# Kernel tuning notes

Measured on AMD Instinct MI355X. Metric: run time of the kernel, lower is better.

## Reference

```python
import jax, jax.numpy as jnp
import numpy as np

K_HOPS = 2  # num_layers in NewSGConv


def setup_inputs() -> dict:
    key = jax.random.key(0)
    ks = jax.random.split(key, 5)
    B, N, F, H, C = 2048, 64, 256, 512, 2
    n_tril = N * (N + 1) // 2  # 2080
    X = jax.random.normal(ks[0], (B, N, F), dtype=jnp.float32)
    edge_weight_tril = jax.random.normal(ks[1], (n_tril,), dtype=jnp.float32) * 0.1
    conv_W = jax.random.normal(ks[2], (F, H), dtype=jnp.float32) * (1.0 / np.sqrt(F))
    conv_b = jnp.zeros((H,), dtype=jnp.float32)
    fc_W = jax.random.normal(ks[3], (C, H), dtype=jnp.float32) * (1.0 / np.sqrt(H))
    fc_b = jnp.zeros((C,), dtype=jnp.float32)
    return {"X": X, "edge_weight_tril": edge_weight_tril, "conv_W": conv_W,
            "conv_b": conv_b, "fc_W": fc_W, "fc_b": fc_b}


def reference(X, edge_weight_tril, conv_W, conv_b, fc_W, fc_b):
    # X: [B, N, F] ; graph is fully connected over N nodes, shared across batch.
    N = X.shape[1]
    xs, ys = jnp.tril_indices(N)
    # Rebuild symmetric dense weight matrix from lower-triangular learnable params
    W = jnp.zeros((N, N), dtype=X.dtype).at[xs, ys].set(edge_weight_tril)
    W = W + W.T - jnp.diag(jnp.diag(W))
    # NewSGConv norm: add self-loops (fill=1), deg from abs(edge_weight)
    A = W + jnp.eye(N, dtype=X.dtype)                 # W_sym + I (extra self-loop edge)
    deg = jnp.abs(W).sum(axis=1) + 1.0                # abs of self-loop weight = 1
    dinv = jnp.where(deg > 0, deg ** -0.5, 0.0)
    An = dinv[:, None] * A * dinv[None, :]            # D^-1/2 (W_sym + I) D^-1/2
    # K-hop SGConv propagation (dense graph -> batched matmul is the exact math)
    x = X
    for _ in range(K_HOPS):
        x = jnp.einsum('nm,bmf->bnf', An, x)
    # SGConv linear, then ReLU (as in model forward)
    h = jax.nn.relu(jnp.einsum('bnf,fh->bnh', x, conv_W) + conv_b)  # [B,N,H]
    # global_add_pool over nodes per graph
    pooled = h.sum(axis=1)                            # [B, H]
    # dropout is identity in eval; final fc + log_softmax
    logits = pooled @ fc_W.T + fc_b                   # [B, C]
    return jax.nn.log_softmax(logits, axis=-1)
```

## Files before the change

### kernel.cpp

```cpp
#include <hip/hip_runtime.h>

typedef float f32x4 __attribute__((ext_vector_type(4)));
typedef short bf16x8 __attribute__((ext_vector_type(8)));

__device__ __forceinline__ short f2bf(float x) {
    unsigned u = __float_as_uint(x);
    unsigned r = (u + 0x7FFFu + ((u >> 16) & 1u)) >> 16;
    return (short)r;
}

__global__ void prep_an2(const float* __restrict__ tril, short* __restrict__ an2f) {
    __shared__ float Wm[64][64];
    __shared__ float An[64][64];
    __shared__ float An2[64][64];
    __shared__ float dinv[64];
    const int t = threadIdx.x;
    for (int e = t; e < 4096; e += 256) {
        int i = e >> 6, j = e & 63;
        int hi = i > j ? i : j, lo = i > j ? j : i;
        Wm[i][j] = tril[hi * (hi + 1) / 2 + lo];
    }
    __syncthreads();
    if (t < 64) {
        float s = 0.f;
        for (int j = 0; j < 64; ++j) s += fabsf(Wm[t][j]);
        s += 1.0f;
        dinv[t] = (s > 0.f) ? 1.0f / sqrtf(s) : 0.f;
    }
    __syncthreads();
    for (int e = t; e < 4096; e += 256) {
        int i = e >> 6, j = e & 63;
        float a = Wm[i][j] + (i == j ? 1.0f : 0.0f);
        An[i][j] = dinv[i] * a * dinv[j];
    }
    __syncthreads();
    for (int e = t; e < 4096; e += 256) {
        int i = e >> 6, j = e & 63;
        float acc = 0.f;
        for (int m = 0; m < 64; ++m) acc += An[i][m] * An[m][j];
        An2[i][j] = acc;
    }
    __syncthreads();
    for (int o = t; o < 4096; o += 256) {
        int e = o & 7, lane = (o >> 3) & 63, kt = (o >> 9) & 1, mt = o >> 10;
        int m = mt * 16 + (lane & 15);
        int k = kt * 32 + 8 * (lane >> 4) + e;
        an2f[o] = f2bf(An2[m][k]);
    }
}

__global__ void prep_wf(const float* __restrict__ convW, short* __restrict__ wf) {
    int o = blockIdx.x * 256 + threadIdx.x;
    int e = o & 7, lane = (o >> 3) & 63, nt = (o >> 9) & 31, kt = o >> 14;
    int k = kt * 32 + 8 * (lane >> 4) + e;
    int j = nt * 16 + (lane & 15);
    wf[o] = f2bf(convW[k * 512 + j]);
}

__global__ __launch_bounds__(256, 2) void rgnn_main(
    const float* __restrict__ X, const short* __restrict__ an2f,
    const short* __restrict__ wf, const float* __restrict__ convb,
    const float* __restrict__ fcW, const float* __restrict__ fcb,
    float* __restrict__ out)
{
    __shared__ short xbuf[16384];
    __shared__ short an2lds[4096];
    __shared__ float pooled[512];
    const int b = blockIdx.x;
    const int t = threadIdx.x;
    const int lane = t & 63;
    const int wid = t >> 6;
    const float* Xb = X + (size_t)b * (64 * 256);

    {
        bf16x8 a0 = *(const bf16x8*)&an2f[t * 16];
        bf16x8 a1 = *(const bf16x8*)&an2f[t * 16 + 8];
        *(bf16x8*)&an2lds[t * 16] = a0;
        *(bf16x8*)&an2lds[t * 16 + 8] = a1;
    }
    {
        const int c = t;
        #pragma unroll 2
        for (int m0 = 0; m0 < 64; m0 += 8) {
            bf16x8 v;
            #pragma unroll
            for (int i = 0; i < 8; ++i) v[i] = f2bf(Xb[(m0 + i) * 256 + c]);
            int byte = c * 128 + m0 * 2;
            byte ^= (c & 7) << 4;
            *(bf16x8*)((char*)xbuf + byte) = v;
        }
    }
    __syncthreads();

    f32x4 acc_a[4][4];
    {
        const int c0 = wid * 64;
        #pragma unroll
        for (int mt = 0; mt < 4; ++mt)
            #pragma unroll
            for (int nt = 0; nt < 4; ++nt) acc_a[mt][nt] = (f32x4)0.f;
        #pragma unroll
        for (int kt = 0; kt < 2; ++kt) {
            #pragma unroll
            for (int nt = 0; nt < 4; ++nt) {
                int row = c0 + nt * 16 + (lane & 15);
                int byte = row * 128 + (kt * 32 + 8 * (lane >> 4)) * 2;
                byte ^= (row & 7) << 4;
                bf16x8 bfr = *(const bf16x8*)((const char*)xbuf + byte);
                #pragma unroll
                for (int mt = 0; mt < 4; ++mt) {
                    bf16x8 afr = *(const bf16x8*)&an2lds[((mt * 2 + kt) * 64 + lane) * 8];
                    acc_a[mt][nt] = __builtin_amdgcn_mfma_f32_16x16x32_bf16(afr, bfr, acc_a[mt][nt], 0, 0, 0);
                }
            }
        }
    }
    __syncthreads();

    {
        const int c0 = wid * 64;
        #pragma unroll
        for (int mt = 0; mt < 4; ++mt)
            #pragma unroll
            for (int nt = 0; nt < 4; ++nt)
                #pragma unroll
                for (int r = 0; r < 4; ++r) {
                    int row = mt * 16 + (lane >> 4) * 4 + r;
                    int col = c0 + nt * 16 + (lane & 15);
                    int byte = row * 512 + col * 2;
                    byte ^= (row & 7) << 4;
                    *(short*)((char*)xbuf + byte) = f2bf(acc_a[mt][nt][r]);
                }
    }
    __syncthreads();

    #pragma unroll 1
    for (int half = 0; half < 2; ++half) {
        const int j0 = wid * 128 + half * 64;
        f32x4 acc[4][4];
        #pragma unroll
        for (int mt = 0; mt < 4; ++mt)
            #pragma unroll
            for (int nt = 0; nt < 4; ++nt) acc[mt][nt] = (f32x4)0.f;
        #pragma unroll
        for (int kt = 0; kt < 8; ++kt) {
            bf16x8 bfr[4];
            #pragma unroll
            for (int nt = 0; nt < 4; ++nt) {
                int ntg = (j0 >> 4) + nt;
                bfr[nt] = *(const bf16x8*)&wf[((kt * 32 + ntg) * 64 + lane) * 8];
            }
            #pragma unroll
            for (int mt = 0; mt < 4; ++mt) {
                int row = mt * 16 + (lane & 15);
                int byte = row * 512 + (kt * 32 + 8 * (lane >> 4)) * 2;
                byte ^= (row & 7) << 4;
                bf16x8 afrb = *(const bf16x8*)((const char*)xbuf + byte);
                #pragma unroll
                for (int nt = 0; nt < 4; ++nt)
                    acc[mt][nt] = __builtin_amdgcn_mfma_f32_16x16x32_bf16(afrb, bfr[nt], acc[mt][nt], 0, 0, 0);
            }
        }
        #pragma unroll
        for (int nt = 0; nt < 4; ++nt) {
            int j = j0 + nt * 16 + (lane & 15);
            float bj = convb[j];
            float s = 0.f;
            #pragma unroll
            for (int mt = 0; mt < 4; ++mt)
                #pragma unroll
                for (int r = 0; r < 4; ++r)
                    s += fmaxf(acc[mt][nt][r] + bj, 0.f);
            s += __shfl_xor(s, 16);
            s += __shfl_xor(s, 32);
            if (lane < 16) pooled[j] = s;
        }
    }
    __syncthreads();

    if (wid == 0) {
        float p0 = 0.f, p1 = 0.f;
        #pragma unroll
        for (int j = lane; j < 512; j += 64) {
            float pv = pooled[j];
            p0 += pv * fcW[j];
            p1 += pv * fcW[512 + j];
        }
        #pragma unroll
        for (int d = 1; d < 64; d <<= 1) {
            p0 += __shfl_xor(p0, d);
            p1 += __shfl_xor(p1, d);
        }
        if (lane == 0) {
            float l0 = p0 + fcb[0], l1 = p1 + fcb[1];
            float m = fmaxf(l0, l1);
            float lse = m + logf(expf(l0 - m) + expf(l1 - m));
            out[b * 2 + 0] = l0 - lse;
            out[b * 2 + 1] = l1 - lse;
        }
    }
}

extern "C" void kernel_launch(void* const* d_in, const int* in_sizes, int n_in,
                              void* d_out, int out_size, void* d_ws, size_t ws_size,
                              hipStream_t stream) {
    const float* X     = (const float*)d_in[0];
    const float* tril  = (const float*)d_in[1];
    const float* convW = (const float*)d_in[2];
    const float* convb = (const float*)d_in[3];
    const float* fcW   = (const float*)d_in[4];
    const float* fcb   = (const float*)d_in[5];
    float* out = (float*)d_out;
    short* an2f = (short*)d_ws;
    short* wf   = an2f + 4096;
    prep_an2<<<dim3(1), dim3(256), 0, stream>>>(tril, an2f);
    prep_wf<<<dim3(512), dim3(256), 0, stream>>>(convW, wf);
    rgnn_main<<<dim3(2048), dim3(256), 0, stream>>>(X, an2f, wf, convb, fcW, fcb, out);
}
```

Measured before the change: 102.2 us.

## Use 512-thread blocks with 8 waves splitting both GEMM stages

Doubles the block size from 256 to 512 threads so eight waves share each graph. The X load is split across two thread halves, the propagation GEMM gives each wave 32 feature columns, and the linear GEMM gives each wave 64 output columns looped over two node halves with a running pooled sum. The aim is more latency hiding and memory-level parallelism per batch element. The cost is that each wave reloads the same weight fragments twice, and register and LDS pressure may limit occupancy.

After: 212.0 us. +107.4%, slower.

```diff
diff --git a/kernel.cpp b/kernel.cpp
--- a/kernel.cpp
+++ b/kernel.cpp
@@ -57,7 +57,7 @@
     wf[o] = f2bf(convW[k * 512 + j]);
 }
 
-__global__ __launch_bounds__(256, 2) void rgnn_main(
+__global__ __launch_bounds__(512, 4) void rgnn_main(
     const float* __restrict__ X, const short* __restrict__ an2f,
     const short* __restrict__ wf, const float* __restrict__ convb,
     const float* __restrict__ fcW, const float* __restrict__ fcb,
@@ -72,57 +72,55 @@
     const int wid = t >> 6;
     const float* Xb = X + (size_t)b * (64 * 256);
 
-    {
-        bf16x8 a0 = *(const bf16x8*)&an2f[t * 16];
-        bf16x8 a1 = *(const bf16x8*)&an2f[t * 16 + 8];
-        *(bf16x8*)&an2lds[t * 16] = a0;
-        *(bf16x8*)&an2lds[t * 16 + 8] = a1;
-    }
-    {
-        const int c = t;
+    *(bf16x8*)&an2lds[t * 8] = *(const bf16x8*)&an2f[t * 8];
+    {
+        const int c = t & 255, mh = t >> 8;
         #pragma unroll 2
-        for (int m0 = 0; m0 < 64; m0 += 8) {
+        for (int m0 = 0; m0 < 32; m0 += 8) {
             bf16x8 v;
             #pragma unroll
-            for (int i = 0; i < 8; ++i) v[i] = f2bf(Xb[(m0 + i) * 256 + c]);
-            int byte = c * 128 + m0 * 2;
+            for (int i = 0; i < 8; ++i) v[i] = f2bf(Xb[(mh * 32 + m0 + i) * 256 + c]);
+            int byte = c * 128 + (mh * 32 + m0) * 2;
             byte ^= (c & 7) << 4;
             *(bf16x8*)((char*)xbuf + byte) = v;
         }
     }
     __syncthreads();
 
-    f32x4 acc_a[4][4];
-    {
-        const int c0 = wid * 64;
-        #pragma unroll
-        for (int mt = 0; mt < 4; ++mt)
-            #pragma unroll
-            for (int nt = 0; nt < 4; ++nt) acc_a[mt][nt] = (f32x4)0.f;
-        #pragma unroll
-        for (int kt = 0; kt < 2; ++kt) {
-            #pragma unroll
-            for (int nt = 0; nt < 4; ++nt) {
+    f32x4 acc_a[4][2];
+    {
+        const int c0 = wid * 32;
+        bf16x8 bfr[2][2];
+        #pragma unroll
+        for (int kt = 0; kt < 2; ++kt)
+            #pragma unroll
+            for (int nt = 0; nt < 2; ++nt) {
                 int row = c0 + nt * 16 + (lane & 15);
                 int byte = row * 128 + (kt * 32 + 8 * (lane >> 4)) * 2;
                 byte ^= (row & 7) << 4;
-                bf16x8 bfr = *(const bf16x8*)((const char*)xbuf + byte);
-                #pragma unroll
-                for (int mt = 0; mt < 4; ++mt) {
-                    bf16x8 afr = *(const bf16x8*)&an2lds[((mt * 2 + kt) * 64 + lane) * 8];
-                    acc_a[mt][nt] = __builtin_amdgcn_mfma_f32_16x16x32_bf16(afr, bfr, acc_a[mt][nt], 0, 0, 0);
-                }
-            }
-        }
-    }
-    __syncthreads();
-
-    {
-        const int c0 = wid * 64;
+                bfr[kt][nt] = *(const bf16x8*)((const char*)xbuf + byte);
+            }
+        #pragma unroll
+        for (int mt = 0; mt < 4; ++mt) {
+            #pragma unroll
+            for (int nt = 0; nt < 2; ++nt) acc_a[mt][nt] = (f32x4)0.f;
+            #pragma unroll
+            for (int kt = 0; kt < 2; ++kt) {
+                bf16x8 afr = *(const bf16x8*)&an2lds[((mt * 2 + kt) * 64 + lane) * 8];
+                #pragma unroll
+                for (int nt = 0; nt < 2; ++nt)
+                    acc_a[mt][nt] = __builtin_amdgcn_mfma_f32_16x16x32_bf16(afr, bfr[kt][nt], acc_a[mt][nt], 0, 0, 0);
+            }
+        }
+    }
+    __syncthreads();
+
+    {
+        const int c0 = wid * 32;
         #pragma unroll
         for (int mt = 0; mt < 4; ++mt)
             #pragma unroll
-            for (int nt = 0; nt < 4; ++nt)
+            for (int nt = 0; nt < 2; ++nt)
                 #pragma unroll
                 for (int r = 0; r < 4; ++r) {
                     int row = mt * 16 + (lane >> 4) * 4 + r;
@@ -134,46 +132,53 @@
     }
     __syncthreads();
 
-    #pragma unroll 1
-    for (int half = 0; half < 2; ++half) {
-        const int j0 = wid * 128 + half * 64;
-        f32x4 acc[4][4];
-        #pragma unroll
-        for (int mt = 0; mt < 4; ++mt)
-            #pragma unroll
-            for (int nt = 0; nt < 4; ++nt) acc[mt][nt] = (f32x4)0.f;
-        #pragma unroll
-        for (int kt = 0; kt < 8; ++kt) {
-            bf16x8 bfr[4];
+    {
+        const int j0 = wid * 64;
+        float psum[4] = {0.f, 0.f, 0.f, 0.f};
+        #pragma unroll 1
+        for (int nh = 0; nh < 2; ++nh) {
+            f32x4 acc[2][4];
+            #pragma unroll
+            for (int mt = 0; mt < 2; ++mt)
+                #pragma unroll
+                for (int nt = 0; nt < 4; ++nt) acc[mt][nt] = (f32x4)0.f;
+            #pragma unroll
+            for (int kt = 0; kt < 8; ++kt) {
+                bf16x8 bw[4];
+                #pragma unroll
+                for (int nt = 0; nt < 4; ++nt) {
+                    int ntg = (j0 >> 4) + nt;
+                    bw[nt] = *(const bf16x8*)&wf[((kt * 32 + ntg) * 64 + lane) * 8];
+                }
+                #pragma unroll
+                for (int mt = 0; mt < 2; ++mt) {
+                    int n = nh * 32 + mt * 16 + (lane & 15);
+                    int byte = n * 512 + (kt * 32 + 8 * (lane >> 4)) * 2;
+                    byte ^= (n & 7) << 4;
+                    bf16x8 ax = *(const bf16x8*)((const char*)xbuf + byte);
+                    #pragma unroll
+                    for (int nt = 0; nt < 4; ++nt)
+                        acc[mt][nt] = __builtin_amdgcn_mfma_f32_16x16x32_bf16(ax, bw[nt], acc[mt][nt], 0, 0, 0);
+                }
+            }
             #pragma unroll
             for (int nt = 0; nt < 4; ++nt) {
-                int ntg = (j0 >> 4) + nt;
-                bfr[nt] = *(const bf16x8*)&wf[((kt * 32 + ntg) * 64 + lane) * 8];
-            }
-            #pragma unroll
-            for (int mt = 0; mt < 4; ++mt) {
-                int row = mt * 16 + (lane & 15);
-                int byte = row * 512 + (kt * 32 + 8 * (lane >> 4)) * 2;
-                byte ^= (row & 7) << 4;
-                bf16x8 afrb = *(const bf16x8*)((const char*)xbuf + byte);
-                #pragma unroll
-                for (int nt = 0; nt < 4; ++nt)
-                    acc[mt][nt] = __builtin_amdgcn_mfma_f32_16x16x32_bf16(afrb, bfr[nt], acc[mt][nt], 0, 0, 0);
+                float bj = convb[j0 + nt * 16 + (lane & 15)];
+                float s = 0.f;
+                #pragma unroll
+                for (int mt = 0; mt < 2; ++mt)
+                    #pragma unroll
+                    for (int r = 0; r < 4; ++r)
+                        s += fmaxf(acc[mt][nt][r] + bj, 0.f);
+                psum[nt] += s;
             }
         }
         #pragma unroll
         for (int nt = 0; nt < 4; ++nt) {
-            int j = j0 + nt * 16 + (lane & 15);
-            float bj = convb[j];
-            float s = 0.f;
-            #pragma unroll
-            for (int mt = 0; mt < 4; ++mt)
-                #pragma unroll
-                for (int r = 0; r < 4; ++r)
-                    s += fmaxf(acc[mt][nt][r] + bj, 0.f);
+            float s = psum[nt];
             s += __shfl_xor(s, 16);
             s += __shfl_xor(s, 32);
-            if (lane < 16) pooled[j] = s;
+            if (lane < 16) pooled[j0 + nt * 16 + (lane & 15)] = s;
         }
     }
     __syncthreads();
@@ -215,5 +220,5 @@
     short* wf   = an2f + 4096;
     prep_an2<<<dim3(1), dim3(256), 0, stream>>>(tril, an2f);
     prep_wf<<<dim3(512), dim3(256), 0, stream>>>(convW, wf);
-    rgnn_main<<<dim3(2048), dim3(256), 0, stream>>>(X, an2f, wf, convb, fcW, fcb, out);
-}
+    rgnn_main<<<dim3(2048), dim3(512), 0, stream>>>(X, an2f, wf, convb, fcW, fcb, out);
+}
```
